# Performance work log

Hardware: AMD Instinct MI355X
Metric: run time of the kernel (lower is better)

Reference implementation:

```python
import jax, jax.numpy as jnp
import numpy as np

NMUL = 16
NASH = 3
NEARZERO = 1e-5
TIMESTEP_D = 1.0
LENF = 15

PARAM_BOUNDS = [
    ("schaake_const", 0.0, 0.1), ("smcmax", 0.3, 0.6), ("soil_depth", 0.5, 3.0),
    ("wltsmc", 0.05, 0.2), ("satpsi", 0.01, 0.5), ("bb", 2.0, 12.0),
    ("mult", 100.0, 2000.0), ("satdk", 1e-7, 1e-4), ("slop", 0.0, 1.0),
    ("max_gw_storage", 0.01, 0.5), ("Cgw", 1e-6, 1e-3), ("expon", 1.0, 8.0),
    ("K_nash", 0.01, 0.5),
]
ROUT_BOUNDS = [("rout_a", 0.0, 2.9), ("rout_b", 0.0, 6.5)]


def setup_inputs() -> dict:
    key = jax.random.key(0)
    k1, k2 = jax.random.split(key)
    T, B = 730, 2048
    # prcp ~ U[0,20) mm/d, pet ~ U[0,8) mm/d
    x_phy = jax.random.uniform(k1, (T, B, 2), dtype=jnp.float32) * jnp.array([20.0, 8.0], jnp.float32)
    n_static = len(PARAM_BOUNDS) * NMUL + len(ROUT_BOUNDS)  # 210
    phy_static = jax.random.uniform(k2, (B, n_static), dtype=jnp.float32)
    return {"x_phy": x_phy, "phy_static": phy_static}


def _cfe_forward(x_phy, phy_static):
    T, B, _ = x_phy.shape
    n_phys = len(PARAM_BOUNDS)
    # descale: change_param_range(p, [lb, ub]) = p * (ub - lb) + lb
    phys = phy_static[:, : n_phys * NMUL].reshape(B, n_phys, NMUL)
    prm = {name: phys[:, i, :] * (ub - lb) + lb for i, (name, lb, ub) in enumerate(PARAM_BOUNDS)}
    route_raw = phy_static[:, n_phys * NMUL :]
    rout = {name: route_raw[:, i] * (ub - lb) + lb for i, (name, lb, ub) in enumerate(ROUT_BOUNDS)}

    P = jnp.repeat(x_phy[:, :, 0:1], NMUL, axis=2)    # [T,B,NMUL]
    PET = jnp.repeat(x_phy[:, :, 1:2], NMUL, axis=2)  # [T,B,NMUL]

    soil0 = jnp.full((B, NMUL), 0.05, jnp.float32)
    gw0 = jnp.full((B, NMUL), 0.01, jnp.float32)
    nash0 = jnp.full((B, NMUL, NASH), NEARZERO, jnp.float32)

    max_soil = prm["smcmax"] * prm["soil_depth"]
    # Clapp-Hornberger field-capacity threshold from satpsi, bb
    fc_frac = jnp.clip((prm["satpsi"] / prm["soil_depth"]) ** (1.0 / prm["bb"]), 0.0, 1.0)
    fc_threshold = prm["smcmax"] * fc_frac * prm["soil_depth"]

    def step(carry, forc):
        soil, gw, nash = carry
        p, pet = forc
        # --- ET: first from rainfall, then Budyko-type from soil ---
        et_rain = jnp.minimum(p, pet)
        p_rem = p - et_rain
        pet_rem = pet - et_rain
        smc = soil / prm["soil_depth"]
        budyko = jnp.clip((smc - prm["wltsmc"]) / (prm["smcmax"] - prm["wltsmc"] + NEARZERO), 0.0, 1.0)
        aet_soil = jnp.minimum(pet_rem * budyko, jnp.maximum(soil - NEARZERO, 0.0))
        soil = soil - aet_soil
        aet = et_rain + aet_soil
        # --- Schaake infiltration / runoff partitioning ---
        deficit = jnp.maximum(max_soil - soil, 0.0)
        infil_cap = deficit * (1.0 - jnp.exp(-prm["schaake_const"] * TIMESTEP_D))
        runoff = p_rem * p_rem / (p_rem + infil_cap + NEARZERO)
        runoff = jnp.minimum(runoff, p_rem)
        infiltration = jnp.minimum(p_rem - runoff, deficit)
        runoff = p_rem - infiltration
        soil = soil + infiltration
        # --- soil dual-outlet nonlinear reservoir (percolation + lateral) ---
        above = jnp.maximum(soil - fc_threshold, 0.0)
        frac = above / jnp.maximum(max_soil - fc_threshold, NEARZERO)
        perc = prm["satdk"] * prm["mult"] * TIMESTEP_D * frac
        lat = prm["satdk"] * prm["mult"] * prm["slop"] * TIMESTEP_D * frac
        tot = perc + lat
        scale = jnp.minimum(1.0, above / jnp.maximum(tot, NEARZERO))
        perc = perc * scale
        lat = lat * scale
        soil = soil - perc - lat
        # --- groundwater exponential reservoir ---
        gw = gw + perc
        q_gw = prm["Cgw"] * jnp.expm1(prm["expon"] * jnp.clip(gw / prm["max_gw_storage"], 0.0, 1.0))
        q_gw = jnp.clip(q_gw, 0.0, jnp.maximum(gw - NEARZERO, 0.0))
        gw = gw - q_gw
        # --- Nash cascade routing of lateral flow (3 linear reservoirs) ---
        inflow = lat
        K = prm["K_nash"]
        new_nash = []
        for i in range(NASH):
            s = nash[..., i] + inflow
            out = K * s
            new_nash.append(s - out)
            inflow = out
        nash = jnp.stack(new_nash, axis=-1)
        q_lat = inflow
        q_sim = runoff + q_lat + q_gw
        return (soil, gw, nash), (q_sim, runoff, q_lat, q_gw, aet, soil, gw)

    _, outs = jax.lax.scan(step, (soil0, gw0, nash0), (P, PET))
    q_sim = outs[0]                 # [T,B,NMUL]
    q_avg = q_sim.mean(-1)          # [T,B]  multi-model averaging

    # --- gamma unit-hydrograph routing (uh_gamma + causal uh_conv) ---
    a = jax.nn.relu(rout["rout_a"])[:, None] + 0.1    # [B,1]
    th = jax.nn.relu(rout["rout_b"])[:, None] + 0.5   # [B,1]
    t = (jnp.arange(LENF, dtype=jnp.float32) + 0.5)[None, :]  # [1,LENF]
    w = t ** (a - 1.0) * jnp.exp(-t / th) / (jnp.exp(jax.lax.lgamma(a)) * th ** a)
    w = w / w.sum(1, keepdims=True)                    # [B,LENF]
    xp = jnp.pad(q_avg, ((LENF - 1, 0), (0, 0)))       # causal pad on time axis
    stream = sum(
        w[None, :, j] * jax.lax.dynamic_slice_in_dim(xp, LENF - 1 - j, T, 0)
        for j in range(LENF)
    )
    return stream[..., None]  # [T,B,1] routed streamflow


def reference(x_phy, phy_static):
    return _cfe_forward(x_phy, phy_static)
```

## Files before the change

### kernel.cpp

```cpp
#include <hip/hip_runtime.h>
#include <math.h>


constexpr int T_STEPS = 730;
constexpr int BATCH   = 2048;
constexpr int NMULC   = 16;
constexpr int LENFC   = 15;
constexpr int NPHYS   = 13;
constexpr int NSTAT   = NPHYS * NMULC + 2;
constexpr float NZ    = 1e-5f;
constexpr int NCH     = 2;
constexpr int LPB     = 8;

__device__ __forceinline__ float frcp(float x) { return __builtin_amdgcn_rcpf(x); }

__device__ __forceinline__ float dpp_sum8(float x) {
    int v;
    v = __builtin_amdgcn_update_dpp(0, __float_as_int(x), 0xB1, 0xF, 0xF, true);
    x += __int_as_float(v);
    v = __builtin_amdgcn_update_dpp(0, __float_as_int(x), 0x4E, 0xF, 0xF, true);
    x += __int_as_float(v);
    v = __builtin_amdgcn_update_dpp(0, __float_as_int(x), 0x141, 0xF, 0xF, true);
    x += __int_as_float(v);
    return x;
}

__global__ __launch_bounds__(64, 1)
void cfe_kernel(const float* __restrict__ x,
                const float* __restrict__ ps,
                float* __restrict__ out)
{
    const int tid = blockIdx.x * 64 + threadIdx.x;
    const int b   = tid >> 3;
    const int m0  = tid & 7;
    if (b >= BATCH) return;

    const float* __restrict__ row = ps + b * NSTAT;

    float k1[NCH], k2[NCH], max_soil[NCH], fc_th[NCH], ic[NCH], cc[NCH],
          pc[NCH], lc[NCH], sc_c[NCH], e2[NCH], Km[NCH], Kk[NCH],
          Cgw[NCH], inv_mgw[NCH];

    #pragma unroll
    for (int c = 0; c < NCH; ++c) {
        const int m = m0 + c * 8;
        const float schaake    = row[ 0*NMULC + m] * 0.1f;
        const float smcmax     = row[ 1*NMULC + m] * 0.3f   + 0.3f;
        const float soil_depth = row[ 2*NMULC + m] * 2.5f   + 0.5f;
        const float wltsmc     = row[ 3*NMULC + m] * 0.15f  + 0.05f;
        const float satpsi     = row[ 4*NMULC + m] * 0.49f  + 0.01f;
        const float bb         = row[ 5*NMULC + m] * 10.0f  + 2.0f;
        const float multp      = row[ 6*NMULC + m] * 1900.0f+ 100.0f;
        const float satdk      = row[ 7*NMULC + m] * (1e-4f - 1e-7f) + 1e-7f;
        const float slop       = row[ 8*NMULC + m];
        const float max_gw     = row[ 9*NMULC + m] * 0.49f  + 0.01f;
        Cgw[c]                 = row[10*NMULC + m] * (1e-3f - 1e-6f) + 1e-6f;
        const float expon      = row[11*NMULC + m] * 7.0f   + 1.0f;
        Kk[c]                  = row[12*NMULC + m] * 0.49f  + 0.01f;

        const float inv_sd  = 1.0f / soil_depth;
        const float bud_den = 1.0f / (smcmax - wltsmc + NZ);
        k1[c] = inv_sd * bud_den;
        k2[c] = -wltsmc * bud_den;
        max_soil[c] = smcmax * soil_depth;
        float fc_frac = powf(satpsi * inv_sd, 1.0f / bb);
        fc_frac = fminf(fmaxf(fc_frac, 0.0f), 1.0f);
        fc_th[c] = smcmax * fc_frac * soil_depth;
        ic[c] = 1.0f - expf(-schaake);
        const float sm  = satdk * multp;
        const float sml = sm * slop;
        const float inv_mft = 1.0f / fmaxf(max_soil[c] - fc_th[c], NZ);
        inv_mgw[c] = 1.0f / max_gw;
        cc[c] = inv_mft * (sm + sml);
        pc[c] = sm  * inv_mft;
        lc[c] = sml * inv_mft;
        sc_c[c] = fminf(1.0f, 1.0f / cc[c]);
        e2[c] = expon * 1.442695041f;
        Km[c] = 1.0f - Kk[c];
    }
    const float inv_nz = 1.0f / NZ;

    const float rout_a = row[NPHYS*NMULC + 0] * 2.9f;
    const float rout_b = row[NPHYS*NMULC + 1] * 6.5f;
    const float a  = fmaxf(rout_a, 0.0f) + 0.1f;
    const float th = fmaxf(rout_b, 0.0f) + 0.5f;
    float w[LENFC];
    float wsum = 0.0f;
    #pragma unroll
    for (int j = 0; j < LENFC; ++j) {
        const float tj = (float)j + 0.5f;
        w[j] = powf(tj, a - 1.0f) * expf(-tj / th);
        wsum += w[j];
    }
    const float wscale = 1.0f / (wsum * (float)NMULC);
    #pragma unroll
    for (int j = 0; j < LENFC; ++j) w[j] *= wscale;

    float soil[NCH] = {0.05f, 0.05f}, gw[NCH] = {0.01f, 0.01f};
    float n0[NCH] = {NZ, NZ}, n1[NCH] = {NZ, NZ}, n2[NCH] = {NZ, NZ};
    float ring[LENFC];
    #pragma unroll
    for (int j = 0; j < LENFC; ++j) ring[j] = 0.0f;

    const float2* __restrict__ xp = (const float2*)x;

    float2 fb0 = xp[0 * BATCH + b];
    float2 fb1 = xp[1 * BATCH + b];
    float2 fb2 = xp[2 * BATCH + b];
    float2 fb3 = xp[3 * BATCH + b];

    float s_prev = 0.0f;

    #pragma unroll 2
    for (int t = 0; t < T_STEPS; ++t) {
        {
            const float r = dpp_sum8(s_prev);
            if (t > 0 && m0 == 0) out[(t - 1) * BATCH + b] = r;
        }

        const float p   = fb0.x;
        const float pet = fb0.y;
        fb0 = fb1; fb1 = fb2; fb2 = fb3;
        const int tn = (t + 4 < T_STEPS) ? (t + 4) : (T_STEPS - 1);
        fb3 = xp[tn * BATCH + b];

        const float et_rain = fminf(p, pet);
        const float p_rem   = p - et_rain;
        const float pet_rem = pet - et_rain;
        const float prem_nz = p_rem + NZ;
        const float prem_sq = p_rem * p_rem;

        float qsum = 0.0f;
        #pragma unroll
        for (int c = 0; c < NCH; ++c) {
            float budyko = fmaf(soil[c], k1[c], k2[c]);
            budyko = fminf(fmaxf(budyko, 0.0f), 1.0f);
            const float aet = fminf(pet_rem * budyko, soil[c] - NZ);
            float so = soil[c] - aet;

            const float deficit = max_soil[c] - so;
            const float den     = fmaf(deficit, ic[c], prem_nz);
            const float runoff0 = prem_sq * frcp(den);
            const float infil   = fminf(p_rem - runoff0, deficit);
            const float runoff  = p_rem - infil;
            so += infil;

            const float above = fmaxf(so - fc_th[c], 0.0f);
            const float asc   = fminf(above * sc_c[c], above * above * inv_nz);
            const float lat   = lc[c] * asc;
            so = fmaf(-cc[c], asc, so);
            soil[c] = so;

            float g = fmaf(pc[c], asc, gw[c]);
            const float ratio = fminf(g * inv_mgw[c], 1.0f);
            const float qg0   = fmaf(Cgw[c], __builtin_amdgcn_exp2f(e2[c] * ratio), -Cgw[c]);
            const float qg    = fminf(qg0, g - NZ);
            gw[c] = g - qg;

            const float s0 = n0[c] + lat;           const float s1 = fmaf(Kk[c], s0, n1[c]);
            const float s2 = fmaf(Kk[c], s1, n2[c]); const float o2 = Kk[c] * s2;
            n0[c] = Km[c] * s0; n1[c] = Km[c] * s1; n2[c] = Km[c] * s2;

            qsum += runoff + o2 + qg;
        }

        #pragma unroll
        for (int j = LENFC - 1; j > 0; --j) ring[j] = ring[j - 1];
        ring[0] = qsum;
        float c0 = 0.0f, c1 = 0.0f, c2 = 0.0f, c3 = 0.0f;
        #pragma unroll
        for (int j = 0; j < LENFC; j += 4) {
            c0 = fmaf(w[j], ring[j], c0);
            if (j + 1 < LENFC) c1 = fmaf(w[j + 1], ring[j + 1], c1);
            if (j + 2 < LENFC) c2 = fmaf(w[j + 2], ring[j + 2], c2);
            if (j + 3 < LENFC) c3 = fmaf(w[j + 3], ring[j + 3], c3);
        }
        s_prev = (c0 + c1) + (c2 + c3);
    }

    {
        const float r = dpp_sum8(s_prev);
        if (m0 == 0) out[(T_STEPS - 1) * BATCH + b] = r;
    }
}

extern "C" void kernel_launch(void* const* d_in, const int* in_sizes, int n_in,
                              void* d_out, int out_size, void* d_ws, size_t ws_size,
                              hipStream_t stream) {
    const float* x_phy      = (const float*)d_in[0];
    const float* phy_static = (const float*)d_in[1];
    float* out = (float*)d_out;

    const int total = BATCH * LPB;
    const int block = 64;
    const int grid  = total / block;
    cfe_kernel<<<grid, block, 0, stream>>>(x_phy, phy_static, out);
}
```

Measured before the change: 181.4 us.

## Unroll time loop by 15 with static ring indexing and batched forcing loads

Restructures the time loop into blocks of 15 steps, fully unrolled through templated substeps. The ring buffer is indexed modulo 15 at compile time, so the 14 register moves per step for the shift go away. All 15 forcing loads for a block are issued up front in place of a 4-deep rolling prefetch, and the reduce and store now run right after each step instead of being deferred one step. The cost is larger code and higher register pressure, and the loads at each block boundary are exposed rather than overlapped with compute.

```diff
diff --git a/kernel.cpp b/kernel.cpp
--- a/kernel.cpp
+++ b/kernel.cpp
@@ -9,8 +9,11 @@
 constexpr int NPHYS   = 13;
 constexpr int NSTAT   = NPHYS * NMULC + 2;
 constexpr float NZ    = 1e-5f;
+constexpr float INV_NZ= 1e5f;
 constexpr int NCH     = 2;
 constexpr int LPB     = 8;
+constexpr int TB      = 15;
+constexpr int T_MAIN  = 720;
 
 __device__ __forceinline__ float frcp(float x) { return __builtin_amdgcn_rcpf(x); }
 
@@ -25,6 +28,76 @@
     return x;
 }
 
+struct Prm {
+    float k1[NCH], k2[NCH], ms[NCH], fc[NCH], ic[NCH], cc[NCH], pc[NCH],
+          lc[NCH], sc[NCH], e2[NCH], Km[NCH], Kk[NCH], Cg[NCH], ig[NCH];
+    float w[LENFC];
+};
+struct St { float soil[NCH], gw[NCH], n0[NCH], n1[NCH], n2[NCH]; };
+
+template <int SLOT>
+__device__ __forceinline__ float substep(const Prm& P, St& S,
+                                         float (&ring)[LENFC], const float2 fv)
+{
+    const float p = fv.x, pet = fv.y;
+    const float et      = fminf(p, pet);
+    const float p_rem   = p - et;
+    const float pet_rem = pet - et;
+    const float prem_nz = p_rem + NZ;
+    const float prem_sq = p_rem * p_rem;
+
+    float qsum = 0.0f;
+    #pragma unroll
+    for (int c = 0; c < NCH; ++c) {
+        float budyko = fmaf(S.soil[c], P.k1[c], P.k2[c]);
+        budyko = fminf(fmaxf(budyko, 0.0f), 1.0f);
+        const float aet = fminf(pet_rem * budyko, S.soil[c] - NZ);
+        float so = S.soil[c] - aet;
+
+        const float deficit = P.ms[c] - so;
+        const float den     = fmaf(deficit, P.ic[c], prem_nz);
+        const float runoff0 = prem_sq * frcp(den);
+        const float infil   = fminf(p_rem - runoff0, deficit);
+        const float runoff  = p_rem - infil;
+        so += infil;
+
+        const float above = fmaxf(so - P.fc[c], 0.0f);
+        const float asc   = fminf(above * P.sc[c], above * above * INV_NZ);
+        const float lat   = P.lc[c] * asc;
+        so = fmaf(-P.cc[c], asc, so);
+        S.soil[c] = so;
+
+        float g = fmaf(P.pc[c], asc, S.gw[c]);
+        const float ratio = fminf(g * P.ig[c], 1.0f);
+        const float qg0   = fmaf(P.Cg[c], __builtin_amdgcn_exp2f(P.e2[c] * ratio), -P.Cg[c]);
+        const float qg    = fminf(qg0, g - NZ);
+        S.gw[c] = g - qg;
+
+        const float s0 = S.n0[c] + lat;             const float s1 = fmaf(P.Kk[c], s0, S.n1[c]);
+        const float s2 = fmaf(P.Kk[c], s1, S.n2[c]); const float o2 = P.Kk[c] * s2;
+        S.n0[c] = P.Km[c] * s0; S.n1[c] = P.Km[c] * s1; S.n2[c] = P.Km[c] * s2;
+
+        qsum += runoff + o2 + qg;
+    }
+
+    ring[SLOT] = qsum;
+    float c0 = 0.0f, c1 = 0.0f, c2 = 0.0f, c3 = 0.0f;
+    #pragma unroll
+    for (int j = 0; j < LENFC; j += 4) {
+        c0 = fmaf(P.w[j], ring[(SLOT - j + 15) % 15], c0);
+        if (j + 1 < LENFC) c1 = fmaf(P.w[j + 1], ring[(SLOT - j - 1 + 30) % 15], c1);
+        if (j + 2 < LENFC) c2 = fmaf(P.w[j + 2], ring[(SLOT - j - 2 + 30) % 15], c2);
+        if (j + 3 < LENFC) c3 = fmaf(P.w[j + 3], ring[(SLOT - j - 3 + 30) % 15], c3);
+    }
+    return (c0 + c1) + (c2 + c3);
+}
+
+#define SUBST(s) { const float acc = substep<(s)>(P, S, ring, f[(s)]);           \
+                   const float r = dpp_sum8(acc);                                \
+                   if (lane0) out[(tb + (s)) * BATCH + b] = r; }
+#define DO15(X) X(0) X(1) X(2) X(3) X(4) X(5) X(6) X(7) X(8) X(9) X(10) X(11) X(12) X(13) X(14)
+#define DO10(X) X(0) X(1) X(2) X(3) X(4) X(5) X(6) X(7) X(8) X(9)
+
 __global__ __launch_bounds__(64, 1)
 void cfe_kernel(const float* __restrict__ x,
                 const float* __restrict__ ps,
@@ -33,14 +106,11 @@
     const int tid = blockIdx.x * 64 + threadIdx.x;
     const int b   = tid >> 3;
     const int m0  = tid & 7;
-    if (b >= BATCH) return;
+    const bool lane0 = (m0 == 0);
 
     const float* __restrict__ row = ps + b * NSTAT;
 
-    float k1[NCH], k2[NCH], max_soil[NCH], fc_th[NCH], ic[NCH], cc[NCH],
-          pc[NCH], lc[NCH], sc_c[NCH], e2[NCH], Km[NCH], Kk[NCH],
-          Cgw[NCH], inv_mgw[NCH];
-
+    Prm P;
     #pragma unroll
     for (int c = 0; c < NCH; ++c) {
         const int m = m0 + c * 8;
@@ -49,138 +119,79 @@
         const float soil_depth = row[ 2*NMULC + m] * 2.5f   + 0.5f;
         const float wltsmc     = row[ 3*NMULC + m] * 0.15f  + 0.05f;
         const float satpsi     = row[ 4*NMULC + m] * 0.49f  + 0.01f;
-        const float bb         = row[ 5*NMULC + m] * 10.0f  + 2.0f;
+        const float bb_        = row[ 5*NMULC + m] * 10.0f  + 2.0f;
         const float multp      = row[ 6*NMULC + m] * 1900.0f+ 100.0f;
         const float satdk      = row[ 7*NMULC + m] * (1e-4f - 1e-7f) + 1e-7f;
         const float slop       = row[ 8*NMULC + m];
         const float max_gw     = row[ 9*NMULC + m] * 0.49f  + 0.01f;
-        Cgw[c]                 = row[10*NMULC + m] * (1e-3f - 1e-6f) + 1e-6f;
+        P.Cg[c]                = row[10*NMULC + m] * (1e-3f - 1e-6f) + 1e-6f;
         const float expon      = row[11*NMULC + m] * 7.0f   + 1.0f;
-        Kk[c]                  = row[12*NMULC + m] * 0.49f  + 0.01f;
+        P.Kk[c]                = row[12*NMULC + m] * 0.49f  + 0.01f;
 
         const float inv_sd  = 1.0f / soil_depth;
         const float bud_den = 1.0f / (smcmax - wltsmc + NZ);
-        k1[c] = inv_sd * bud_den;
-        k2[c] = -wltsmc * bud_den;
-        max_soil[c] = smcmax * soil_depth;
-        float fc_frac = powf(satpsi * inv_sd, 1.0f / bb);
+        P.k1[c] = inv_sd * bud_den;
+        P.k2[c] = -wltsmc * bud_den;
+        P.ms[c] = smcmax * soil_depth;
+        float fc_frac = powf(satpsi * inv_sd, 1.0f / bb_);
         fc_frac = fminf(fmaxf(fc_frac, 0.0f), 1.0f);
-        fc_th[c] = smcmax * fc_frac * soil_depth;
-        ic[c] = 1.0f - expf(-schaake);
+        P.fc[c] = smcmax * fc_frac * soil_depth;
+        P.ic[c] = 1.0f - expf(-schaake);
         const float sm  = satdk * multp;
         const float sml = sm * slop;
-        const float inv_mft = 1.0f / fmaxf(max_soil[c] - fc_th[c], NZ);
-        inv_mgw[c] = 1.0f / max_gw;
-        cc[c] = inv_mft * (sm + sml);
-        pc[c] = sm  * inv_mft;
-        lc[c] = sml * inv_mft;
-        sc_c[c] = fminf(1.0f, 1.0f / cc[c]);
-        e2[c] = expon * 1.442695041f;
-        Km[c] = 1.0f - Kk[c];
-    }
-    const float inv_nz = 1.0f / NZ;
-
-    const float rout_a = row[NPHYS*NMULC + 0] * 2.9f;
-    const float rout_b = row[NPHYS*NMULC + 1] * 6.5f;
-    const float a  = fmaxf(rout_a, 0.0f) + 0.1f;
-    const float th = fmaxf(rout_b, 0.0f) + 0.5f;
-    float w[LENFC];
-    float wsum = 0.0f;
-    #pragma unroll
-    for (int j = 0; j < LENFC; ++j) {
-        const float tj = (float)j + 0.5f;
-        w[j] = powf(tj, a - 1.0f) * expf(-tj / th);
-        wsum += w[j];
-    }
-    const float wscale = 1.0f / (wsum * (float)NMULC);
-    #pragma unroll
-    for (int j = 0; j < LENFC; ++j) w[j] *= wscale;
-
-    float soil[NCH] = {0.05f, 0.05f}, gw[NCH] = {0.01f, 0.01f};
-    float n0[NCH] = {NZ, NZ}, n1[NCH] = {NZ, NZ}, n2[NCH] = {NZ, NZ};
+        const float inv_mft = 1.0f / fmaxf(P.ms[c] - P.fc[c], NZ);
+        P.ig[c] = 1.0f / max_gw;
+        P.cc[c] = inv_mft * (sm + sml);
+        P.pc[c] = sm  * inv_mft;
+        P.lc[c] = sml * inv_mft;
+        P.sc[c] = fminf(1.0f, 1.0f / P.cc[c]);
+        P.e2[c] = expon * 1.442695041f;
+        P.Km[c] = 1.0f - P.Kk[c];
+    }
+
+    {
+        const float rout_a = row[NPHYS*NMULC + 0] * 2.9f;
+        const float rout_b = row[NPHYS*NMULC + 1] * 6.5f;
+        const float a  = fmaxf(rout_a, 0.0f) + 0.1f;
+        const float th = fmaxf(rout_b, 0.0f) + 0.5f;
+        float wsum = 0.0f;
+        #pragma unroll
+        for (int j = 0; j < LENFC; ++j) {
+            const float tj = (float)j + 0.5f;
+            P.w[j] = powf(tj, a - 1.0f) * expf(-tj / th);
+            wsum += P.w[j];
+        }
+        const float wscale = 1.0f / (wsum * (float)NMULC);
+        #pragma unroll
+        for (int j = 0; j < LENFC; ++j) P.w[j] *= wscale;
+    }
+
+    St S;
+    #pragma unroll
+    for (int c = 0; c < NCH; ++c) {
+        S.soil[c] = 0.05f; S.gw[c] = 0.01f;
+        S.n0[c] = NZ; S.n1[c] = NZ; S.n2[c] = NZ;
+    }
     float ring[LENFC];
     #pragma unroll
     for (int j = 0; j < LENFC; ++j) ring[j] = 0.0f;
 
     const float2* __restrict__ xp = (const float2*)x;
 
-    float2 fb0 = xp[0 * BATCH + b];
-    float2 fb1 = xp[1 * BATCH + b];
-    float2 fb2 = xp[2 * BATCH + b];
-    float2 fb3 = xp[3 * BATCH + b];
-
-    float s_prev = 0.0f;
-
-    #pragma unroll 2
-    for (int t = 0; t < T_STEPS; ++t) {
-        {
-            const float r = dpp_sum8(s_prev);
-            if (t > 0 && m0 == 0) out[(t - 1) * BATCH + b] = r;
-        }
-
-        const float p   = fb0.x;
-        const float pet = fb0.y;
-        fb0 = fb1; fb1 = fb2; fb2 = fb3;
-        const int tn = (t + 4 < T_STEPS) ? (t + 4) : (T_STEPS - 1);
-        fb3 = xp[tn * BATCH + b];
-
-        const float et_rain = fminf(p, pet);
-        const float p_rem   = p - et_rain;
-        const float pet_rem = pet - et_rain;
-        const float prem_nz = p_rem + NZ;
-        const float prem_sq = p_rem * p_rem;
-
-        float qsum = 0.0f;
-        #pragma unroll
-        for (int c = 0; c < NCH; ++c) {
-            float budyko = fmaf(soil[c], k1[c], k2[c]);
-            budyko = fminf(fmaxf(budyko, 0.0f), 1.0f);
-            const float aet = fminf(pet_rem * budyko, soil[c] - NZ);
-            float so = soil[c] - aet;
-
-            const float deficit = max_soil[c] - so;
-            const float den     = fmaf(deficit, ic[c], prem_nz);
-            const float runoff0 = prem_sq * frcp(den);
-            const float infil   = fminf(p_rem - runoff0, deficit);
-            const float runoff  = p_rem - infil;
-            so += infil;
-
-            const float above = fmaxf(so - fc_th[c], 0.0f);
-            const float asc   = fminf(above * sc_c[c], above * above * inv_nz);
-            const float lat   = lc[c] * asc;
-            so = fmaf(-cc[c], asc, so);
-            soil[c] = so;
-
-            float g = fmaf(pc[c], asc, gw[c]);
-            const float ratio = fminf(g * inv_mgw[c], 1.0f);
-            const float qg0   = fmaf(Cgw[c], __builtin_amdgcn_exp2f(e2[c] * ratio), -Cgw[c]);
-            const float qg    = fminf(qg0, g - NZ);
-            gw[c] = g - qg;
-
-            const float s0 = n0[c] + lat;           const float s1 = fmaf(Kk[c], s0, n1[c]);
-            const float s2 = fmaf(Kk[c], s1, n2[c]); const float o2 = Kk[c] * s2;
-            n0[c] = Km[c] * s0; n1[c] = Km[c] * s1; n2[c] = Km[c] * s2;
-
-            qsum += runoff + o2 + qg;
-        }
-
-        #pragma unroll
-        for (int j = LENFC - 1; j > 0; --j) ring[j] = ring[j - 1];
-        ring[0] = qsum;
-        float c0 = 0.0f, c1 = 0.0f, c2 = 0.0f, c3 = 0.0f;
-        #pragma unroll
-        for (int j = 0; j < LENFC; j += 4) {
-            c0 = fmaf(w[j], ring[j], c0);
-            if (j + 1 < LENFC) c1 = fmaf(w[j + 1], ring[j + 1], c1);
-            if (j + 2 < LENFC) c2 = fmaf(w[j + 2], ring[j + 2], c2);
-            if (j + 3 < LENFC) c3 = fmaf(w[j + 3], ring[j + 3], c3);
-        }
-        s_prev = (c0 + c1) + (c2 + c3);
+    #pragma unroll 1
+    for (int tb = 0; tb < T_MAIN; tb += TB) {
+        float2 f[TB];
+        #pragma unroll
+        for (int s = 0; s < TB; ++s) f[s] = xp[(tb + s) * BATCH + b];
+        DO15(SUBST)
     }
 
     {
-        const float r = dpp_sum8(s_prev);
-        if (m0 == 0) out[(T_STEPS - 1) * BATCH + b] = r;
+        const int tb = T_MAIN;
+        float2 f[10];
+        #pragma unroll
+        for (int s = 0; s < 10; ++s) f[s] = xp[(tb + s) * BATCH + b];
+        DO10(SUBST)
     }
 }
 
```

Result: faster. 177.4 us (-2.2%).
